# Performance work log

Measured on AMD Instinct MI355X. Metric: run time of the kernel, lower is better.

Reference implementation:

```python
import jax, jax.numpy as jnp
import numpy as np
from jax import lax

DIM, D_INNER, D_STATE, D_CONV, DT_RANK = 256, 512, 16, 4, 16
B_, H_, W_ = 4, 64, 64


def setup_inputs() -> dict:
    key = jax.random.key(0)
    ks = jax.random.split(key, 10)
    s = lambda k, shape, scale: (jax.random.normal(k, shape, dtype=jnp.float32) * scale)
    inp = {
        "x": s(ks[0], (B_, DIM, H_, W_), 1.0),
        "in_proj_w": s(ks[1], (2 * D_INNER, DIM), DIM ** -0.5),
        "conv_w": s(ks[2], (D_INNER, 1, D_CONV), D_CONV ** -0.5),
        "conv_b": s(ks[3], (D_INNER,), 0.02),
        "x_proj_w": s(ks[4], (DT_RANK + 2 * D_STATE, D_INNER), D_INNER ** -0.5),
        "dt_proj_w": s(ks[5], (D_INNER, DT_RANK), DT_RANK ** -0.5),
        "dt_proj_b": s(ks[6], (D_INNER,), 0.02),
        # A_log init: log(arange(1..d_state)) broadcast over channels (standard S4D-real init)
        "A_log": jnp.broadcast_to(jnp.log(jnp.arange(1, D_STATE + 1, dtype=jnp.float32)), (D_INNER, D_STATE)).copy(),
        "D": jnp.ones((D_INNER,), dtype=jnp.float32),
        "out_proj_w": s(ks[7], (DIM, D_INNER), D_INNER ** -0.5),
    }
    return inp


def _mamba_forward(x, in_proj_w, conv_w, conv_b, x_proj_w, dt_proj_w, dt_proj_b, A_log, D, out_proj_w):
    b, c, h, w = x.shape
    L = h * w
    xs = x.reshape(b, c, L).transpose(0, 2, 1)                      # [b, L, dim]

    xz = jnp.einsum('bld,ed->ble', xs, in_proj_w)                   # [b, L, 2*d_inner]
    u, res = jnp.split(xz, 2, axis=-1)                              # each [b, L, d_inner]

    # causal depthwise conv1d over sequence
    u_t = u.transpose(0, 2, 1)                                      # [b, d_inner, L]
    u_t = lax.conv_general_dilated(u_t, conv_w, window_strides=(1,),
                                   padding=[(D_CONV - 1, 0)],
                                   feature_group_count=D_INNER,
                                   dimension_numbers=('NCH', 'OIH', 'NCH'))
    u = jax.nn.silu(u_t.transpose(0, 2, 1) + conv_b)                # [b, L, d_inner]

    dbc = jnp.einsum('bld,ed->ble', u, x_proj_w)                    # [b, L, dt_rank+2n]
    dt, Bm, Cm = jnp.split(dbc, [DT_RANK, DT_RANK + D_STATE], axis=-1)
    delta = jax.nn.softplus(jnp.einsum('blr,dr->bld', dt, dt_proj_w) + dt_proj_b)  # [b,L,d_inner]

    A = -jnp.exp(A_log)                                             # [d_inner, n]
    deltaA = jnp.exp(jnp.einsum('bld,dn->bldn', delta, A))          # [b,L,d,n]
    deltaBu = jnp.einsum('bld,bln,bld->bldn', delta, Bm, u)         # [b,L,d,n]

    def step(state, inp):
        dA, dBu, c_t = inp                                          # [b,d,n],[b,d,n],[b,n]
        state = dA * state + dBu
        y = jnp.einsum('bdn,bn->bd', state, c_t)
        return state, y

    init = jnp.zeros((b, D_INNER, D_STATE), dtype=x.dtype)
    _, ys = lax.scan(step, init, (jnp.moveaxis(deltaA, 1, 0),
                                  jnp.moveaxis(deltaBu, 1, 0),
                                  jnp.moveaxis(Cm, 1, 0)))
    y = jnp.moveaxis(ys, 0, 1) + u * D                              # [b, L, d_inner]
    y = y * jax.nn.silu(res)
    out = jnp.einsum('ble,de->bld', y, out_proj_w)                  # [b, L, dim]
    return out.transpose(0, 2, 1).reshape(b, c, h, w)


def reference(x, in_proj_w, conv_w, conv_b, x_proj_w, dt_proj_w, dt_proj_b, A_log, D, out_proj_w):
    return _mamba_forward(x, in_proj_w, conv_w, conv_b, x_proj_w, dt_proj_w, dt_proj_b, A_log, D, out_proj_w)
```

## Files before the change

kernel.cpp:

```cpp
#include <hip/hip_runtime.h>
#include <math.h>


namespace {
constexpr int kB   = 4;
constexpr int kDim = 256;
constexpr int kL   = 4096;
constexpr int kDI  = 512;
constexpr int kN   = 16;
constexpr int kNC  = 64;
constexpr int kCS  = 64;
}

typedef __attribute__((ext_vector_type(8))) short bf16x8;
typedef __attribute__((ext_vector_type(4))) float f32x4;
typedef __attribute__((ext_vector_type(2))) float f32x2;

__device__ __forceinline__ float rcpf(float x) { return __builtin_amdgcn_rcpf(x); }
__device__ __forceinline__ float siluf(float x) { return x * rcpf(1.f + __expf(-x)); }
__device__ __forceinline__ float softplusf(float x) {
  return fmaxf(x, 0.f) + __logf(1.f + __expf(-fabsf(x)));
}

__device__ __forceinline__ unsigned short f2bf(float x) {
  union { float f; unsigned int u; } v; v.f = x;
  unsigned int u = v.u;
  u += 0x7fffu + ((u >> 16) & 1u);
  return (unsigned short)(u >> 16);
}
__device__ __forceinline__ float bf2f(unsigned short u) {
  union { unsigned int i; float f; } v; v.i = ((unsigned int)u) << 16; return v.f;
}

__device__ __forceinline__ void gload_lds16(const void* g, void* l) {
  __builtin_amdgcn_global_load_lds(
      (const __attribute__((address_space(1))) unsigned int*)g,
      (__attribute__((address_space(3))) unsigned int*)l, 16, 0, 0);
}

__global__ __launch_bounds__(256) void k_prep(const float* __restrict__ w_in,
                                              const float* __restrict__ w_out,
                                              const float* __restrict__ w_x,
                                              const float* __restrict__ w_dt,
                                              const float* __restrict__ A_log,
                                              const float* __restrict__ x,
                                              unsigned short* __restrict__ wib,
                                              unsigned short* __restrict__ wob,
                                              unsigned short* __restrict__ wxb,
                                              unsigned short* __restrict__ wdtb,
                                              float* __restrict__ Avz,
                                              unsigned int* __restrict__ flagA,
                                              unsigned short* __restrict__ xt) {
  __shared__ float Xs[64][65];
  const int blk = blockIdx.x;
  const int t = threadIdx.x;
  if (blk < 1760) {
    int idx = blk * 256 + t;
    if (idx < 262144) wib[idx] = f2bf(w_in[idx]);
    else if (idx < 393216) wob[idx - 262144] = f2bf(w_out[idx - 262144]);
    else if (idx < 417792) wxb[idx - 393216] = f2bf(w_x[idx - 393216]);
    else {
      int i = idx - 417792;
      int r = i & 31, d = i >> 5;
      wdtb[i] = (r < 16) ? f2bf(w_dt[d * 16 + r]) : (unsigned short)0;
    }
  } else if (blk < 1762) {
    int d = (blk - 1760) * 256 + t;
    float a0 = -__expf(A_log[d * kN]);
    bool ok = true;
#pragma unroll
    for (int n = 1; n < kN; ++n) {
      float av = -__expf(A_log[d * kN + n]);
      ok = ok && (fabsf(av - (n + 1) * a0) <= 1e-5f * fabsf(av));
    }
    Avz[d] = a0;
    unsigned long long bal = __ballot(ok);
    int wv = t >> 6;
    if ((t & 63) == 0) ((unsigned long long*)Xs)[wv] = bal;
    __syncthreads();
    if (t == 0) {
      unsigned long long all = ~0ull;
#pragma unroll
      for (int w = 0; w < 4; ++w) all &= ((unsigned long long*)Xs)[w];
      flagA[blk - 1760] = (all == ~0ull) ? 1u : 0u;
    }
  } else {
    int id = blk - 1762;
    int lb = id & 63, db = (id >> 6) & 3, b = id >> 8;
    const int d0 = db * 64, l0 = lb * 64, l = t & 63;
#pragma unroll
    for (int rep = 0; rep < 16; ++rep) {
      int dd = rep * 4 + (t >> 6);
      Xs[dd][l] = x[((size_t)b * kDim + d0 + dd) * kL + l0 + l];
    }
    __syncthreads();
#pragma unroll
    for (int rep = 0; rep < 8; ++rep) {
      int lj = rep * 8 + (t >> 5);
      int di = (t & 31) * 2;
      ushort2 v;
      v.x = f2bf(Xs[di][lj]);
      v.y = f2bf(Xs[di + 1][lj]);
      *(ushort2*)(xt + ((size_t)b * kL + l0 + lj) * kDim + d0 + di) = v;
    }
  }
}

__global__ __launch_bounds__(256) void gemm_in_lm(const unsigned short* __restrict__ xt,
                                                  const unsigned short* __restrict__ W,
                                                  unsigned short* __restrict__ ubf,
                                                  unsigned short* __restrict__ resb) {
  __shared__ __align__(16) unsigned short As[128 * 64];
  __shared__ __align__(16) unsigned short Bs[128 * 64];
  const int e0 = blockIdx.x * 128;
  const int l0 = blockIdx.y * 128;
  const int b  = blockIdx.z;
  const int t  = threadIdx.x;
  const int wave = t >> 6, lane = t & 63;
  const int wm = wave >> 1, wn = wave & 1;
  const unsigned short* Ab = xt + (size_t)b * kL * kDim;

  f32x4 acc[4][4];
#pragma unroll
  for (int i = 0; i < 4; ++i)
#pragma unroll
    for (int j = 0; j < 4; ++j) acc[i][j] = (f32x4)0.0f;

  const int srow = t >> 3, sch = t & 7;
  for (int kt = 0; kt < 4; ++kt) {
    const int k0 = kt * 64;
#pragma unroll
    for (int c = 0; c < 4; ++c) {
      int row = c * 32 + srow;
      int gch = sch ^ (row & 7);
      gload_lds16(Ab + (size_t)(l0 + row) * kDim + k0 + gch * 8,
                  (char*)As + c * 4096 + wave * 1024);
      gload_lds16(W  + (size_t)(e0 + row) * kDim + k0 + gch * 8,
                  (char*)Bs + c * 4096 + wave * 1024);
    }
    __syncthreads();
#pragma unroll
    for (int ks = 0; ks < 2; ++ks) {
      bf16x8 af[4], bfr[4];
#pragma unroll
      for (int f = 0; f < 4; ++f) {
        int ra = wm * 64 + f * 16 + (lane & 15);
        int ca = (ks * 4 + (lane >> 4)) ^ (ra & 7);
        af[f] = *(const bf16x8*)((const char*)As + ra * 128 + ca * 16);
        int rb = wn * 64 + f * 16 + (lane & 15);
        int cb = (ks * 4 + (lane >> 4)) ^ (rb & 7);
        bfr[f] = *(const bf16x8*)((const char*)Bs + rb * 128 + cb * 16);
      }
#pragma unroll
      for (int i = 0; i < 4; ++i)
#pragma unroll
        for (int j = 0; j < 4; ++j)
          acc[i][j] = __builtin_amdgcn_mfma_f32_16x16x32_bf16(af[i], bfr[j], acc[i][j], 0, 0, 0);
    }
    __syncthreads();
  }

  const bool is_u = (e0 < kDI);
  unsigned short* dst = is_u ? ubf : resb;
  const int ebase = is_u ? e0 : (e0 - kDI);
#pragma unroll
  for (int i = 0; i < 4; ++i)
#pragma unroll
    for (int j = 0; j < 4; ++j)
#pragma unroll
      for (int r = 0; r < 4; ++r) {
        int l = l0 + wm * 64 + i * 16 + (lane >> 4) * 4 + r;
        int e = ebase + wn * 64 + j * 16 + (lane & 15);
        dst[((size_t)b * kL + l) * kDI + e] = f2bf(acc[i][j][r]);
      }
}

__global__ __launch_bounds__(256) void k_conv(const unsigned short* __restrict__ ubf,
                                              const float* __restrict__ cw,
                                              const float* __restrict__ cb,
                                              unsigned short* __restrict__ ucb) {
  int idx = blockIdx.x * 256 + threadIdx.x;
  int d8 = idx & 63;
  int l  = (idx >> 6) & (kL - 1);
  int b  = idx >> 18;
  int d0 = d8 * 8;
  const unsigned short* row = ubf + ((size_t)b * kL + l) * kDI + d0;
  uint4 zero = make_uint4(0, 0, 0, 0);
  uint4 c0 = *(const uint4*)row;
  uint4 c1 = (l >= 1) ? *(const uint4*)(row - kDI)     : zero;
  uint4 c2 = (l >= 2) ? *(const uint4*)(row - 2 * kDI) : zero;
  uint4 c3 = (l >= 3) ? *(const uint4*)(row - 3 * kDI) : zero;
  const unsigned int* p0 = (const unsigned int*)&c0;
  const unsigned int* p1 = (const unsigned int*)&c1;
  const unsigned int* p2 = (const unsigned int*)&c2;
  const unsigned int* p3 = (const unsigned int*)&c3;
  unsigned short ov[8];
#pragma unroll
  for (int c = 0; c < 8; ++c) {
    int q = c >> 1, hi = c & 1;
    float u0 = bf2f((unsigned short)(hi ? (p0[q] >> 16) : (p0[q] & 0xffff)));
    float u1 = bf2f((unsigned short)(hi ? (p1[q] >> 16) : (p1[q] & 0xffff)));
    float u2 = bf2f((unsigned short)(hi ? (p2[q] >> 16) : (p2[q] & 0xffff)));
    float u3 = bf2f((unsigned short)(hi ? (p3[q] >> 16) : (p3[q] & 0xffff)));
    float4 w = *(const float4*)(cw + (d0 + c) * 4);
    float acc = cb[d0 + c] + w.x * u3 + w.y * u2 + w.z * u1 + w.w * u0;
    ov[c] = f2bf(siluf(acc));
  }
  *(uint4*)(ucb + ((size_t)b * kL + l) * kDI + d0) = *(const uint4*)ov;
}

__global__ __launch_bounds__(256) void k_xproj_dt(const unsigned short* __restrict__ Wx,
                                                  const unsigned short* __restrict__ Wdtb,
                                                  const float* __restrict__ bdt,
                                                  float* __restrict__ dbcBC,
                                                  const unsigned short* __restrict__ ucb,
                                                  unsigned short* __restrict__ delb) {
  __shared__ __align__(16) unsigned short As[64 * 64];
  __shared__ __align__(16) unsigned short Bs[64 * 64];
  __shared__ __align__(16) unsigned short dtTl[64 * 32];
  __shared__ __align__(16) unsigned short Wl[128 * 32];
  const int l0 = blockIdx.x * 64;
  const int b  = blockIdx.y;
  const int t  = threadIdx.x;
  const int wave = t >> 6, lane = t & 63;
  const unsigned short* Bb = ucb + (size_t)b * kL * kDI;

  f32x4 acc[3];
#pragma unroll
  for (int i = 0; i < 3; ++i) acc[i] = (f32x4)0.0f;

  const int srow = t >> 3, sch = t & 7;
  for (int kt = 0; kt < 8; ++kt) {
    const int k0 = kt * 64;
#pragma unroll
    for (int c = 0; c < 2; ++c) {
      int row = c * 32 + srow;
      int grow = row < 48 ? row : 47;
      int gch = sch ^ (row & 7);
      gload_lds16(Wx + (size_t)grow * kDI + k0 + gch * 8,
                  (char*)As + c * 4096 + wave * 1024);
    }
#pragma unroll
    for (int c = 0; c < 2; ++c) {
      int row = c * 32 + srow;
      int gch = sch ^ (row & 7);
      gload_lds16(Bb + (size_t)(l0 + row) * kDI + k0 + gch * 8,
                  (char*)Bs + c * 4096 + wave * 1024);
    }
    __syncthreads();
#pragma unroll
    for (int ks = 0; ks < 2; ++ks) {
      bf16x8 af[3], bfr;
#pragma unroll
      for (int f = 0; f < 3; ++f) {
        int ra = f * 16 + (lane & 15);
        int ca = (ks * 4 + (lane >> 4)) ^ (ra & 7);
        af[f] = *(const bf16x8*)((const char*)As + ra * 128 + ca * 16);
      }
      int rb = wave * 16 + (lane & 15);
      int cb = (ks * 4 + (lane >> 4)) ^ (rb & 7);
      bfr = *(const bf16x8*)((const char*)Bs + rb * 128 + cb * 16);
#pragma unroll
      for (int i = 0; i < 3; ++i)
        acc[i] = __builtin_amdgcn_mfma_f32_16x16x32_bf16(af[i], bfr, acc[i], 0, 0, 0);
    }
    __syncthreads();
  }

#pragma unroll
  for (int i = 1; i < 3; ++i)
#pragma unroll
    for (int r = 0; r < 4; ++r) {
      int m = i * 16 + (lane >> 4) * 4 + r;
      int l = l0 + wave * 16 + (lane & 15);
      dbcBC[((size_t)b * 32 + (m - 16)) * kL + l] = acc[i][r];
    }
  {
    int lloc = wave * 16 + (lane & 15);
    int m0 = (lane >> 4) * 4;
    ushort4 v;
    v.x = f2bf(acc[0][0]); v.y = f2bf(acc[0][1]);
    v.z = f2bf(acc[0][2]); v.w = f2bf(acc[0][3]);
    int byte = lloc * 64 + (((m0 >> 3) ^ (lloc & 3)) << 4) + ((m0 & 7) << 1);
    *(ushort4*)((char*)dtTl + byte) = v;
  }
  if (t < 128) {
    int lz = t >> 1, zc = 2 + (t & 1);
    *(uint4*)((char*)dtTl + lz * 64 + ((zc ^ (lz & 3)) << 4)) = make_uint4(0, 0, 0, 0);
  }
  __syncthreads();

  for (int dt4 = 0; dt4 < 4; ++dt4) {
#pragma unroll
    for (int c2 = 0; c2 < 2; ++c2) {
      int unit = c2 * 256 + t;
      int row = unit >> 2, sc = unit & 3;
      int gch = sc ^ (row & 3);
      gload_lds16(Wdtb + (size_t)(dt4 * 128 + row) * 32 + gch * 8,
                  (char*)Wl + c2 * 4096 + t * 16);
    }
    __syncthreads();
    f32x4 acc2[4][2];
#pragma unroll
    for (int i = 0; i < 4; ++i)
#pragma unroll
      for (int j = 0; j < 2; ++j) acc2[i][j] = (f32x4)0.0f;
    bf16x8 afr[4], bfr2[2];
#pragma unroll
    for (int f = 0; f < 4; ++f) {
      int ra = f * 16 + (lane & 15);
      afr[f] = *(const bf16x8*)((const char*)dtTl + ra * 64 + (((lane >> 4) ^ (ra & 3)) << 4));
    }
#pragma unroll
    for (int f = 0; f < 2; ++f) {
      int rb = wave * 32 + f * 16 + (lane & 15);
      bfr2[f] = *(const bf16x8*)((const char*)Wl + rb * 64 + (((lane >> 4) ^ (rb & 3)) << 4));
    }
#pragma unroll
    for (int i = 0; i < 4; ++i)
#pragma unroll
      for (int j = 0; j < 2; ++j)
        acc2[i][j] = __builtin_amdgcn_mfma_f32_16x16x32_bf16(afr[i], bfr2[j], acc2[i][j], 0, 0, 0);
#pragma unroll
    for (int j = 0; j < 2; ++j) {
      int d = dt4 * 128 + wave * 32 + j * 16 + (lane & 15);
      float bd = bdt[d];
#pragma unroll
      for (int i = 0; i < 4; ++i)
#pragma unroll
        for (int r = 0; r < 4; ++r) {
          int l = l0 + i * 16 + (lane >> 4) * 4 + r;
          float delta = softplusf(acc2[i][j][r] + bd);
          delb[((size_t)b * kL + l) * kDI + d] = f2bf(delta);
        }
    }
    __syncthreads();
  }
}

__global__ __launch_bounds__(128) void k_scanA(const unsigned short* __restrict__ delb,
                                               const unsigned short* __restrict__ ucb,
                                               const float* __restrict__ dbcBC,
                                               const float* __restrict__ A_log,
                                               const float* __restrict__ Avz,
                                               const unsigned int* __restrict__ flagA,
                                               float* __restrict__ Pprod,
                                               float* __restrict__ Pfull,
                                               float* __restrict__ S) {
  __shared__ __align__(16) float Bsh[16][kCS];
  const int b = blockIdx.z, ch = blockIdx.y;
  const int t = threadIdx.x;
  const int d = blockIdx.x * 128 + t;
  const int l0 = ch * kCS;
  {
    int row = t >> 3, li = (t & 7) * 8;
    *(float4*)&Bsh[row][li] =
        *(const float4*)&dbcBC[((size_t)b * 32 + row) * kL + l0 + li];
    *(float4*)&Bsh[row][li + 4] =
        *(const float4*)&dbcBC[((size_t)b * 32 + row) * kL + l0 + li + 4];
  }
  __syncthreads();
  const bool fast = (flagA[0] != 0u) && (flagA[1] != 0u);
  const float Av0 = Avz[d];
  const unsigned short* pDel = delb + ((size_t)b * kL + l0) * kDI + d;
  const unsigned short* pU = ucb + ((size_t)b * kL + l0) * kDI + d;
  size_t obase = (size_t)(b * kNC + ch) * (kN * kDI) + d;

  if (fast) {
    f32x2 Sv2[8];
#pragma unroll
    for (int m = 0; m < 8; ++m) Sv2[m] = (f32x2){0.f, 0.f};
    float Pp = 1.f;
    for (int i = 0; i < kCS; i += 4) {
      f32x2 a2[4], e2[4], du2[4];
#pragma unroll
      for (int jj = 0; jj < 4; ++jj) {
        float dl = bf2f(pDel[(size_t)(i + jj) * kDI]);
        float uu = bf2f(pU[(size_t)(i + jj) * kDI]);
        float E = __expf(dl * Av0);
        float duv = dl * uu;
        du2[jj] = (f32x2){duv, duv};
        float Esq = E * E;
        a2[jj] = (f32x2){E, Esq};
        e2[jj] = (f32x2){Esq, Esq};
        Pp *= E;
      }
#pragma unroll
      for (int m = 0; m < 8; ++m) {
        float4 Ba = *(const float4*)&Bsh[2 * m][i];
        float4 Bb = *(const float4*)&Bsh[2 * m + 1][i];
        Sv2[m] = Sv2[m] * a2[0] + du2[0] * (f32x2){Ba.x, Bb.x};
        Sv2[m] = Sv2[m] * a2[1] + du2[1] * (f32x2){Ba.y, Bb.y};
        Sv2[m] = Sv2[m] * a2[2] + du2[2] * (f32x2){Ba.z, Bb.z};
        Sv2[m] = Sv2[m] * a2[3] + du2[3] * (f32x2){Ba.w, Bb.w};
        if (m < 7) {
          a2[0] *= e2[0]; a2[1] *= e2[1]; a2[2] *= e2[2]; a2[3] *= e2[3];
        }
      }
    }
    Pprod[(size_t)(b * kNC + ch) * kDI + d] = Pp;
#pragma unroll
    for (int n = 0; n < kN; ++n)
      S[obase + (size_t)n * kDI] = (n & 1) ? Sv2[n >> 1].y : Sv2[n >> 1].x;
  } else {
    float Av[16];
#pragma unroll
    for (int n = 0; n < kN; ++n) Av[n] = -__expf(A_log[d * kN + n]);
    float Pv[16], Sv[16];
#pragma unroll
    for (int n = 0; n < kN; ++n) { Pv[n] = 1.f; Sv[n] = 0.f; }
    for (int i = 0; i < kCS; i += 4) {
      float del[4], du[4];
#pragma unroll
      for (int jj = 0; jj < 4; ++jj) {
        del[jj] = bf2f(pDel[(size_t)(i + jj) * kDI]);
        du[jj] = del[jj] * bf2f(pU[(size_t)(i + jj) * kDI]);
      }
#pragma unroll
      for (int n = 0; n < kN; ++n) {
        float4 B4 = *(const float4*)&Bsh[n][i];
        float a;
        a = __expf(del[0] * Av[n]); Pv[n] *= a; Sv[n] = Sv[n] * a + du[0] * B4.x;
        a = __expf(del[1] * Av[n]); Pv[n] *= a; Sv[n] = Sv[n] * a + du[1] * B4.y;
        a = __expf(del[2] * Av[n]); Pv[n] *= a; Sv[n] = Sv[n] * a + du[2] * B4.z;
        a = __expf(del[3] * Av[n]); Pv[n] *= a; Sv[n] = Sv[n] * a + du[3] * B4.w;
      }
    }
#pragma unroll
    for (int n = 0; n < kN; ++n) {
      Pfull[obase + (size_t)n * kDI] = Pv[n];
      S[obase + (size_t)n * kDI] = Sv[n];
    }
  }
}

__global__ __launch_bounds__(64) void k_scanB(const float* __restrict__ Pprod,
                                              const float* __restrict__ Pfull,
                                              const float* __restrict__ S,
                                              const unsigned int* __restrict__ flagA,
                                              float* __restrict__ init) {
  int idx = blockIdx.x * 64 + threadIdx.x;
  int b = idx >> 13, nd = idx & 8191;
  int n = nd >> 9, d = nd & 511;
  size_t base = (size_t)b * kNC * 8192 + nd;
  const bool fast = (flagA[0] != 0u) && (flagA[1] != 0u);
  float carry = 0.f;
  if (fast) {
    size_t pbase = (size_t)b * kNC * kDI + d;
    const int e = n + 1;
    for (int c0 = 0; c0 < kNC; c0 += 8) {
      float p[8], s[8];
#pragma unroll
      for (int j = 0; j < 8; ++j) {
        float pr = Pprod[pbase + (size_t)(c0 + j) * kDI];
        float p2 = pr * pr, p4 = p2 * p2, p8 = p4 * p4;
        float pw = 1.f;
        if (e & 1) pw *= pr;
        if (e & 2) pw *= p2;
        if (e & 4) pw *= p4;
        if (e & 8) pw *= p8;
        if (e & 16) pw *= p8 * p8;
        p[j] = pw;
        s[j] = S[base + (size_t)(c0 + j) * 8192];
      }
#pragma unroll
      for (int j = 0; j < 8; ++j) {
        init[base + (size_t)(c0 + j) * 8192] = carry;
        carry = p[j] * carry + s[j];
      }
    }
  } else {
    for (int c0 = 0; c0 < kNC; c0 += 8) {
      float p[8], s[8];
#pragma unroll
      for (int j = 0; j < 8; ++j) {
        size_t o = base + (size_t)(c0 + j) * 8192;
        p[j] = Pfull[o]; s[j] = S[o];
      }
#pragma unroll
      for (int j = 0; j < 8; ++j) {
        init[base + (size_t)(c0 + j) * 8192] = carry;
        carry = p[j] * carry + s[j];
      }
    }
  }
}

__global__ __launch_bounds__(128) void k_scanC(const unsigned short* __restrict__ delb,
                                               const unsigned short* __restrict__ ucb,
                                               const float* __restrict__ dbcBC,
                                               const float* __restrict__ A_log,
                                               const float* __restrict__ Avz,
                                               const unsigned int* __restrict__ flagA,
                                               const float* __restrict__ init,
                                               const unsigned short* __restrict__ resb,
                                               const float* __restrict__ Dp,
                                               unsigned short* __restrict__ yt) {
  __shared__ __align__(16) float BCsh[32][kCS];
  const int b = blockIdx.z, ch = blockIdx.y;
  const int t = threadIdx.x;
  const int d = blockIdx.x * 128 + t;
  const int l0 = ch * kCS;
  {
    int row = t >> 2, li = (t & 3) * 16;
#pragma unroll
    for (int q = 0; q < 4; ++q)
      *(float4*)&BCsh[row][li + q * 4] =
          *(const float4*)&dbcBC[((size_t)b * 32 + row) * kL + l0 + li + q * 4];
  }
  __syncthreads();
  const bool fast = (flagA[0] != 0u) && (flagA[1] != 0u);
  const float Av0 = Avz[d];
  const float Dv = Dp[d];
  const unsigned short* pDel = delb + ((size_t)b * kL + l0) * kDI + d;
  const unsigned short* pU = ucb + ((size_t)b * kL + l0) * kDI + d;
  const unsigned short* pR = resb + ((size_t)b * kL + l0) * kDI + d;
  unsigned short* pY = yt + ((size_t)b * kL + l0) * kDI + d;
  size_t ibase = (size_t)(b * kNC + ch) * (kN * kDI) + d;

  if (fast) {
    f32x2 s2[8];
#pragma unroll
    for (int m = 0; m < 8; ++m)
      s2[m] = (f32x2){init[ibase + (size_t)(2 * m) * kDI],
                      init[ibase + (size_t)(2 * m + 1) * kDI]};
    for (int i = 0; i < kCS; i += 4) {
      float uv[4];
      f32x2 a2[4], e2[4], du2[4], yacc2[4];
#pragma unroll
      for (int jj = 0; jj < 4; ++jj) {
        float dl = bf2f(pDel[(size_t)(i + jj) * kDI]);
        uv[jj] = bf2f(pU[(size_t)(i + jj) * kDI]);
        float E = __expf(dl * Av0);
        float duv = dl * uv[jj];
        du2[jj] = (f32x2){duv, duv};
        float Esq = E * E;
        a2[jj] = (f32x2){E, Esq};
        e2[jj] = (f32x2){Esq, Esq};
        yacc2[jj] = (f32x2){0.f, 0.f};
      }
#pragma unroll
      for (int m = 0; m < 8; ++m) {
        float4 Ba = *(const float4*)&BCsh[2 * m][i];
        float4 Bb = *(const float4*)&BCsh[2 * m + 1][i];
        float4 Ca = *(const float4*)&BCsh[16 + 2 * m][i];
        float4 Cb = *(const float4*)&BCsh[16 + 2 * m + 1][i];
        s2[m] = s2[m] * a2[0] + du2[0] * (f32x2){Ba.x, Bb.x};
        yacc2[0] = yacc2[0] + s2[m] * (f32x2){Ca.x, Cb.x};
        s2[m] = s2[m] * a2[1] + du2[1] * (f32x2){Ba.y, Bb.y};
        yacc2[1] = yacc2[1] + s2[m] * (f32x2){Ca.y, Cb.y};
        s2[m] = s2[m] * a2[2] + du2[2] * (f32x2){Ba.z, Bb.z};
        yacc2[2] = yacc2[2] + s2[m] * (f32x2){Ca.z, Cb.z};
        s2[m] = s2[m] * a2[3] + du2[3] * (f32x2){Ba.w, Bb.w};
        yacc2[3] = yacc2[3] + s2[m] * (f32x2){Ca.w, Cb.w};
        if (m < 7) {
          a2[0] *= e2[0]; a2[1] *= e2[1]; a2[2] *= e2[2]; a2[3] *= e2[3];
        }
      }
#pragma unroll
      for (int jj = 0; jj < 4; ++jj) {
        float yv = yacc2[jj].x + yacc2[jj].y;
        float r = bf2f(pR[(size_t)(i + jj) * kDI]);
        float gv = (yv + uv[jj] * Dv) * siluf(r);
        pY[(size_t)(i + jj) * kDI] = f2bf(gv);
      }
    }
  } else {
    float Av[16];
#pragma unroll
    for (int n = 0; n < kN; ++n) Av[n] = -__expf(A_log[d * kN + n]);
    float s[16];
#pragma unroll
    for (int n = 0; n < kN; ++n) s[n] = init[ibase + (size_t)n * kDI];
    for (int i = 0; i < kCS; i += 4) {
      float uv[4], du[4], del[4], yacc[4] = {0.f, 0.f, 0.f, 0.f};
#pragma unroll
      for (int jj = 0; jj < 4; ++jj) {
        del[jj] = bf2f(pDel[(size_t)(i + jj) * kDI]);
        uv[jj] = bf2f(pU[(size_t)(i + jj) * kDI]);
        du[jj] = del[jj] * uv[jj];
      }
#pragma unroll
      for (int n = 0; n < kN; ++n) {
        float4 B4 = *(const float4*)&BCsh[n][i];
        float4 C4 = *(const float4*)&BCsh[16 + n][i];
        float a;
        a = __expf(del[0] * Av[n]); s[n] = s[n] * a + du[0] * B4.x; yacc[0] += s[n] * C4.x;
        a = __expf(del[1] * Av[n]); s[n] = s[n] * a + du[1] * B4.y; yacc[1] += s[n] * C4.y;
        a = __expf(del[2] * Av[n]); s[n] = s[n] * a + du[2] * B4.z; yacc[2] += s[n] * C4.z;
        a = __expf(del[3] * Av[n]); s[n] = s[n] * a + du[3] * B4.w; yacc[3] += s[n] * C4.w;
      }
#pragma unroll
      for (int jj = 0; jj < 4; ++jj) {
        float r = bf2f(pR[(size_t)(i + jj) * kDI]);
        float gv = (yacc[jj] + uv[jj] * Dv) * siluf(r);
        pY[(size_t)(i + jj) * kDI] = f2bf(gv);
      }
    }
  }
}

__global__ __launch_bounds__(256) void gemm_out(const unsigned short* __restrict__ A,
                                                const unsigned short* __restrict__ Bt,
                                                float* __restrict__ C0) {
  __shared__ __align__(16) unsigned short As[128 * 64];
  __shared__ __align__(16) unsigned short Bs[128 * 64];
  const int n0 = blockIdx.x * 128;
  const int m0 = blockIdx.y * 128;
  const int b  = blockIdx.z;
  const int t  = threadIdx.x;
  const int wave = t >> 6, lane = t & 63;
  const int wm = wave >> 1, wn = wave & 1;
  const unsigned short* Bb = Bt + (size_t)b * kL * kDI;

  f32x4 acc[4][4];
#pragma unroll
  for (int i = 0; i < 4; ++i)
#pragma unroll
    for (int j = 0; j < 4; ++j) acc[i][j] = (f32x4)0.0f;

  const int srow = t >> 3, sch = t & 7;
  for (int kt = 0; kt < 8; ++kt) {
    const int k0 = kt * 64;
#pragma unroll
    for (int c = 0; c < 4; ++c) {
      int row = c * 32 + srow;
      int gch = sch ^ (row & 7);
      gload_lds16(A  + (size_t)(m0 + row) * kDI + k0 + gch * 8,
                  (char*)As + c * 4096 + wave * 1024);
      gload_lds16(Bb + (size_t)(n0 + row) * kDI + k0 + gch * 8,
                  (char*)Bs + c * 4096 + wave * 1024);
    }
    __syncthreads();
#pragma unroll
    for (int ks = 0; ks < 2; ++ks) {
      bf16x8 af[4], bfr[4];
#pragma unroll
      for (int f = 0; f < 4; ++f) {
        int ra = wm * 64 + f * 16 + (lane & 15);
        int ca = (ks * 4 + (lane >> 4)) ^ (ra & 7);
        af[f] = *(const bf16x8*)((const char*)As + ra * 128 + ca * 16);
        int rb = wn * 64 + f * 16 + (lane & 15);
        int cb = (ks * 4 + (lane >> 4)) ^ (rb & 7);
        bfr[f] = *(const bf16x8*)((const char*)Bs + rb * 128 + cb * 16);
      }
#pragma unroll
      for (int i = 0; i < 4; ++i)
#pragma unroll
        for (int j = 0; j < 4; ++j)
          acc[i][j] = __builtin_amdgcn_mfma_f32_16x16x32_bf16(af[i], bfr[j], acc[i][j], 0, 0, 0);
    }
    __syncthreads();
  }
#pragma unroll
  for (int i = 0; i < 4; ++i)
#pragma unroll
    for (int j = 0; j < 4; ++j)
#pragma unroll
      for (int r = 0; r < 4; ++r) {
        int m = m0 + wm * 64 + i * 16 + (lane >> 4) * 4 + r;
        int n = n0 + wn * 64 + j * 16 + (lane & 15);
        C0[((size_t)b * kDim + m) * kL + n] = acc[i][j][r];
      }
}

extern "C" void kernel_launch(void* const* d_in, const int* in_sizes, int n_in,
                              void* d_out, int out_size, void* d_ws, size_t ws_size,
                              hipStream_t stream) {
  const float* x       = (const float*)d_in[0];
  const float* in_w    = (const float*)d_in[1];
  const float* conv_w  = (const float*)d_in[2];
  const float* conv_b  = (const float*)d_in[3];
  const float* xproj_w = (const float*)d_in[4];
  const float* dt_w    = (const float*)d_in[5];
  const float* dt_b    = (const float*)d_in[6];
  const float* A_log   = (const float*)d_in[7];
  const float* Dp      = (const float*)d_in[8];
  const float* out_w   = (const float*)d_in[9];
  float* out = (float*)d_out;

  float* ws = (float*)d_ws;
  const size_t nBLD  = (size_t)kB * kL * kDI;
  const size_t nPS   = (size_t)kB * kNC * kN * kDI;
  float* dbcBC  = ws;
  float* Sb     = dbcBC + 524288;
  float* initb  = Sb + nPS;
  float* Pprodb = initb + nPS;
  unsigned short* ubf  = (unsigned short*)(Pprodb + 131072);
  unsigned short* ucb  = ubf + nBLD;
  unsigned short* resb = ucb + nBLD;
  unsigned short* delb = resb + nBLD;
  unsigned short* wib  = delb + nBLD;
  unsigned short* wob  = wib + 262144;
  unsigned short* wxb  = wob + 131072;
  unsigned short* wdtb = wxb + 24576;
  float* Avz           = (float*)(wdtb + 32768);
  unsigned int* flagA  = (unsigned int*)(Avz + 512);
  unsigned short* xt   = delb;
  float* Pfull         = (float*)ubf;
  unsigned short* yt   = (unsigned short*)ubf;

  k_prep<<<dim3(2786), 256, 0, stream>>>(in_w, out_w, xproj_w, dt_w, A_log, x,
                                         wib, wob, wxb, wdtb, Avz, flagA, xt);
  gemm_in_lm<<<dim3(8, kL / 128, kB), 256, 0, stream>>>(xt, wib, ubf, resb);
  k_conv<<<dim3((unsigned)(kB * kL * 64 / 256)), 256, 0, stream>>>(ubf, conv_w, conv_b, ucb);
  k_xproj_dt<<<dim3(kL / 64, kB), 256, 0, stream>>>(wxb, wdtb, dt_b, dbcBC, ucb, delb);
  k_scanA<<<dim3(4, kNC, kB), 128, 0, stream>>>(delb, ucb, dbcBC, A_log, Avz, flagA, Pprodb, Pfull, Sb);
  k_scanB<<<dim3(kB * kDI * kN / 64), 64, 0, stream>>>(Pprodb, Pfull, Sb, flagA, initb);
  k_scanC<<<dim3(4, kNC, kB), 128, 0, stream>>>(delb, ucb, dbcBC, A_log, Avz, flagA, initb, resb, Dp, yt);
  gemm_out<<<dim3(kL / 128, kDim / 128, kB), 256, 0, stream>>>(wob, yt, out);
}
```

Before: 141.6 us.

## Fuse chunk-local scan pass into x_proj/dt kernel using shared-memory delta and B tiles

After: 150.3 us. 6.1% more time.

```diff
diff --git a/kernel.cpp b/kernel.cpp
--- a/kernel.cpp
+++ b/kernel.cpp
@@ -10,6 +10,7 @@
 constexpr int kN   = 16;
 constexpr int kNC  = 64;
 constexpr int kCS  = 64;
+constexpr int kDP  = 520;
 }
 
 typedef __attribute__((ext_vector_type(8))) short bf16x8;
@@ -209,17 +210,27 @@
   *(uint4*)(ucb + ((size_t)b * kL + l) * kDI + d0) = *(const uint4*)ov;
 }
 
-__global__ __launch_bounds__(256) void k_xproj_dt(const unsigned short* __restrict__ Wx,
-                                                  const unsigned short* __restrict__ Wdtb,
-                                                  const float* __restrict__ bdt,
-                                                  float* __restrict__ dbcBC,
-                                                  const unsigned short* __restrict__ ucb,
-                                                  unsigned short* __restrict__ delb) {
+__global__ __launch_bounds__(256) void k_xproj_dt_scanA(
+    const unsigned short* __restrict__ Wx,
+    const unsigned short* __restrict__ Wdtb,
+    const float* __restrict__ bdt,
+    float* __restrict__ dbcBC,
+    const unsigned short* __restrict__ ucb,
+    unsigned short* __restrict__ delb,
+    const float* __restrict__ A_log,
+    const float* __restrict__ Avz,
+    const unsigned int* __restrict__ flagA,
+    float* __restrict__ Pprod,
+    float* __restrict__ Pfull,
+    float* __restrict__ S) {
   __shared__ __align__(16) unsigned short As[64 * 64];
   __shared__ __align__(16) unsigned short Bs[64 * 64];
   __shared__ __align__(16) unsigned short dtTl[64 * 32];
   __shared__ __align__(16) unsigned short Wl[128 * 32];
+  __shared__ __align__(16) float BshA[16][68];
+  __shared__ __align__(16) unsigned short delTl[64 * kDP];
   const int l0 = blockIdx.x * 64;
+  const int ch = blockIdx.x;
   const int b  = blockIdx.y;
   const int t  = threadIdx.x;
   const int wave = t >> 6, lane = t & 63;
@@ -277,6 +288,11 @@
     }
   {
     int lloc = wave * 16 + (lane & 15);
+#pragma unroll
+    for (int r = 0; r < 4; ++r) {
+      int n = (lane >> 4) * 4 + r;
+      BshA[n][lloc] = acc[1][r];
+    }
     int m0 = (lane >> 4) * 4;
     ushort4 v;
     v.x = f2bf(acc[0][0]); v.y = f2bf(acc[0][1]);
@@ -329,107 +345,86 @@
       for (int i = 0; i < 4; ++i)
 #pragma unroll
         for (int r = 0; r < 4; ++r) {
-          int l = l0 + i * 16 + (lane >> 4) * 4 + r;
+          int lloc = i * 16 + (lane >> 4) * 4 + r;
           float delta = softplusf(acc2[i][j][r] + bd);
-          delb[((size_t)b * kL + l) * kDI + d] = f2bf(delta);
+          unsigned short dv = f2bf(delta);
+          delb[((size_t)b * kL + l0 + lloc) * kDI + d] = dv;
+          delTl[lloc * kDP + d] = dv;
         }
     }
     __syncthreads();
   }
-}
-
-__global__ __launch_bounds__(128) void k_scanA(const unsigned short* __restrict__ delb,
-                                               const unsigned short* __restrict__ ucb,
-                                               const float* __restrict__ dbcBC,
-                                               const float* __restrict__ A_log,
-                                               const float* __restrict__ Avz,
-                                               const unsigned int* __restrict__ flagA,
-                                               float* __restrict__ Pprod,
-                                               float* __restrict__ Pfull,
-                                               float* __restrict__ S) {
-  __shared__ __align__(16) float Bsh[16][kCS];
-  const int b = blockIdx.z, ch = blockIdx.y;
-  const int t = threadIdx.x;
-  const int d = blockIdx.x * 128 + t;
-  const int l0 = ch * kCS;
-  {
-    int row = t >> 3, li = (t & 7) * 8;
-    *(float4*)&Bsh[row][li] =
-        *(const float4*)&dbcBC[((size_t)b * 32 + row) * kL + l0 + li];
-    *(float4*)&Bsh[row][li + 4] =
-        *(const float4*)&dbcBC[((size_t)b * 32 + row) * kL + l0 + li + 4];
-  }
-  __syncthreads();
+
   const bool fast = (flagA[0] != 0u) && (flagA[1] != 0u);
-  const float Av0 = Avz[d];
-  const unsigned short* pDel = delb + ((size_t)b * kL + l0) * kDI + d;
-  const unsigned short* pU = ucb + ((size_t)b * kL + l0) * kDI + d;
-  size_t obase = (size_t)(b * kNC + ch) * (kN * kDI) + d;
-
-  if (fast) {
-    f32x2 Sv2[8];
-#pragma unroll
-    for (int m = 0; m < 8; ++m) Sv2[m] = (f32x2){0.f, 0.f};
-    float Pp = 1.f;
-    for (int i = 0; i < kCS; i += 4) {
-      f32x2 a2[4], e2[4], du2[4];
-#pragma unroll
-      for (int jj = 0; jj < 4; ++jj) {
-        float dl = bf2f(pDel[(size_t)(i + jj) * kDI]);
-        float uu = bf2f(pU[(size_t)(i + jj) * kDI]);
-        float E = __expf(dl * Av0);
-        float duv = dl * uu;
-        du2[jj] = (f32x2){duv, duv};
-        float Esq = E * E;
-        a2[jj] = (f32x2){E, Esq};
-        e2[jj] = (f32x2){Esq, Esq};
-        Pp *= E;
-      }
-#pragma unroll
-      for (int m = 0; m < 8; ++m) {
-        float4 Ba = *(const float4*)&Bsh[2 * m][i];
-        float4 Bb = *(const float4*)&Bsh[2 * m + 1][i];
-        Sv2[m] = Sv2[m] * a2[0] + du2[0] * (f32x2){Ba.x, Bb.x};
-        Sv2[m] = Sv2[m] * a2[1] + du2[1] * (f32x2){Ba.y, Bb.y};
-        Sv2[m] = Sv2[m] * a2[2] + du2[2] * (f32x2){Ba.z, Bb.z};
-        Sv2[m] = Sv2[m] * a2[3] + du2[3] * (f32x2){Ba.w, Bb.w};
-        if (m < 7) {
-          a2[0] *= e2[0]; a2[1] *= e2[1]; a2[2] *= e2[2]; a2[3] *= e2[3];
+  for (int half = 0; half < 2; ++half) {
+    const int dd = half * 256 + t;
+    const float Av0 = Avz[dd];
+    const unsigned short* pU = ucb + ((size_t)b * kL + l0) * kDI + dd;
+    size_t obase = (size_t)(b * kNC + ch) * (kN * kDI) + dd;
+    if (fast) {
+      f32x2 Sv2[8];
+#pragma unroll
+      for (int m = 0; m < 8; ++m) Sv2[m] = (f32x2){0.f, 0.f};
+      float Pp = 1.f;
+      for (int i = 0; i < kCS; i += 4) {
+        f32x2 a2[4], e2[4], du2[4];
+#pragma unroll
+        for (int jj = 0; jj < 4; ++jj) {
+          float dl = bf2f(delTl[(i + jj) * kDP + dd]);
+          float uu = bf2f(pU[(size_t)(i + jj) * kDI]);
+          float E = __expf(dl * Av0);
+          float duv = dl * uu;
+          du2[jj] = (f32x2){duv, duv};
+          float Esq = E * E;
+          a2[jj] = (f32x2){E, Esq};
+          e2[jj] = (f32x2){Esq, Esq};
+          Pp *= E;
         }
-      }
-    }
-    Pprod[(size_t)(b * kNC + ch) * kDI + d] = Pp;
-#pragma unroll
-    for (int n = 0; n < kN; ++n)
-      S[obase + (size_t)n * kDI] = (n & 1) ? Sv2[n >> 1].y : Sv2[n >> 1].x;
-  } else {
-    float Av[16];
-#pragma unroll
-    for (int n = 0; n < kN; ++n) Av[n] = -__expf(A_log[d * kN + n]);
-    float Pv[16], Sv[16];
-#pragma unroll
-    for (int n = 0; n < kN; ++n) { Pv[n] = 1.f; Sv[n] = 0.f; }
-    for (int i = 0; i < kCS; i += 4) {
-      float del[4], du[4];
-#pragma unroll
-      for (int jj = 0; jj < 4; ++jj) {
-        del[jj] = bf2f(pDel[(size_t)(i + jj) * kDI]);
-        du[jj] = del[jj] * bf2f(pU[(size_t)(i + jj) * kDI]);
+#pragma unroll
+        for (int m = 0; m < 8; ++m) {
+          float4 Ba = *(const float4*)&BshA[2 * m][i];
+          float4 Bb2 = *(const float4*)&BshA[2 * m + 1][i];
+          Sv2[m] = Sv2[m] * a2[0] + du2[0] * (f32x2){Ba.x, Bb2.x};
+          Sv2[m] = Sv2[m] * a2[1] + du2[1] * (f32x2){Ba.y, Bb2.y};
+          Sv2[m] = Sv2[m] * a2[2] + du2[2] * (f32x2){Ba.z, Bb2.z};
+          Sv2[m] = Sv2[m] * a2[3] + du2[3] * (f32x2){Ba.w, Bb2.w};
+          if (m < 7) {
+            a2[0] *= e2[0]; a2[1] *= e2[1]; a2[2] *= e2[2]; a2[3] *= e2[3];
+          }
+        }
+      }
+      Pprod[(size_t)(b * kNC + ch) * kDI + dd] = Pp;
+#pragma unroll
+      for (int n = 0; n < kN; ++n)
+        S[obase + (size_t)n * kDI] = (n & 1) ? Sv2[n >> 1].y : Sv2[n >> 1].x;
+    } else {
+      float Av[16];
+#pragma unroll
+      for (int n = 0; n < kN; ++n) Av[n] = -__expf(A_log[dd * kN + n]);
+      float Pv[16], Sv[16];
+#pragma unroll
+      for (int n = 0; n < kN; ++n) { Pv[n] = 1.f; Sv[n] = 0.f; }
+      for (int i = 0; i < kCS; i += 4) {
+        float del[4], du[4];
+#pragma unroll
+        for (int jj = 0; jj < 4; ++jj) {
+          del[jj] = bf2f(delTl[(i + jj) * kDP + dd]);
+          du[jj] = del[jj] * bf2f(pU[(size_t)(i + jj) * kDI]);
+        }
+#pragma unroll
+        for (int n = 0; n < kN; ++n) {
+          float a;
+          a = __expf(del[0] * Av[n]); Pv[n] *= a; Sv[n] = Sv[n] * a + du[0] * BshA[n][i + 0];
+          a = __expf(del[1] * Av[n]); Pv[n] *= a; Sv[n] = Sv[n] * a + du[1] * BshA[n][i + 1];
+          a = __expf(del[2] * Av[n]); Pv[n] *= a; Sv[n] = Sv[n] * a + du[2] * BshA[n][i + 2];
+          a = __expf(del[3] * Av[n]); Pv[n] *= a; Sv[n] = Sv[n] * a + du[3] * BshA[n][i + 3];
+        }
       }
 #pragma unroll
       for (int n = 0; n < kN; ++n) {
-        float4 B4 = *(const float4*)&Bsh[n][i];
-        float a;
-        a = __expf(del[0] * Av[n]); Pv[n] *= a; Sv[n] = Sv[n] * a + du[0] * B4.x;
-        a = __expf(del[1] * Av[n]); Pv[n] *= a; Sv[n] = Sv[n] * a + du[1] * B4.y;
-        a = __expf(del[2] * Av[n]); Pv[n] *= a; Sv[n] = Sv[n] * a + du[2] * B4.z;
-        a = __expf(del[3] * Av[n]); Pv[n] *= a; Sv[n] = Sv[n] * a + du[3] * B4.w;
-      }
-    }
-#pragma unroll
-    for (int n = 0; n < kN; ++n) {
-      Pfull[obase + (size_t)n * kDI] = Pv[n];
-      S[obase + (size_t)n * kDI] = Sv[n];
+        Pfull[obase + (size_t)n * kDI] = Pv[n];
+        S[obase + (size_t)n * kDI] = Sv[n];
+      }
     }
   }
 }
@@ -704,8 +699,8 @@
                                          wib, wob, wxb, wdtb, Avz, flagA, xt);
   gemm_in_lm<<<dim3(8, kL / 128, kB), 256, 0, stream>>>(xt, wib, ubf, resb);
   k_conv<<<dim3((unsigned)(kB * kL * 64 / 256)), 256, 0, stream>>>(ubf, conv_w, conv_b, ucb);
-  k_xproj_dt<<<dim3(kL / 64, kB), 256, 0, stream>>>(wxb, wdtb, dt_b, dbcBC, ucb, delb);
-  k_scanA<<<dim3(4, kNC, kB), 128, 0, stream>>>(delb, ucb, dbcBC, A_log, Avz, flagA, Pprodb, Pfull, Sb);
+  k_xproj_dt_scanA<<<dim3(kL / 64, kB), 256, 0, stream>>>(wxb, wdtb, dt_b, dbcBC, ucb, delb,
+                                                          A_log, Avz, flagA, Pprodb, Pfull, Sb);
   k_scanB<<<dim3(kB * kDI * kN / 64), 64, 0, stream>>>(Pprodb, Pfull, Sb, flagA, initb);
   k_scanC<<<dim3(4, kNC, kB), 128, 0, stream>>>(delb, ucb, dbcBC, A_log, Avz, flagA, initb, resb, Dp, yt);
   gemm_out<<<dim3(kL / 128, kDim / 128, kB), 256, 0, stream>>>(wob, yt, out);
```
